# Kernel tuning notes

Measured on AMD Instinct MI355X. Metric: run time of the kernel, lower is better.

## Reference

```python
import jax, jax.numpy as jnp
import numpy as np

B, S, E = 2, 2048, 2048
H, W = 16, 256  # num_heads, window_size
D = E // H      # head_dim = 128


def setup_inputs() -> dict:
    key = jax.random.key(0)
    ks = jax.random.split(key, 9)
    s = 1.0 / np.sqrt(E)
    return {
        "x": jax.random.normal(ks[0], (B, S, E), dtype=jnp.float32),
        "Wq": jax.random.normal(ks[1], (E, E), dtype=jnp.float32) * s,
        "bq": jax.random.normal(ks[2], (E,), dtype=jnp.float32) * 0.01,
        "Wk": jax.random.normal(ks[3], (E, E), dtype=jnp.float32) * s,
        "bk": jax.random.normal(ks[4], (E,), dtype=jnp.float32) * 0.01,
        "Wv": jax.random.normal(ks[5], (E, E), dtype=jnp.float32) * s,
        "bv": jax.random.normal(ks[6], (E,), dtype=jnp.float32) * 0.01,
        "Wo": jax.random.normal(ks[7], (E, E), dtype=jnp.float32) * s,
        "bo": jax.random.normal(ks[8], (E,), dtype=jnp.float32) * 0.01,
    }


def reference(x, Wq, bq, Wk, bk, Wv, bv, Wo, bo):
    Bsz, Sl, _ = x.shape
    # projections -> [B, H, S, D]
    def proj(Wt, bt):
        return (x @ Wt + bt).reshape(Bsz, Sl, H, D).transpose(0, 2, 1, 3)
    q = proj(Wq, bq)
    k = proj(Wk, bk)
    v = proj(Wv, bv)
    # scores [B, H, S, S]
    scores = jnp.einsum("bhqd,bhkd->bhqk", q, k) / jnp.sqrt(jnp.float32(D))
    # causal sliding-window mask: q_pos - W < k_pos <= q_pos
    q_pos = jnp.arange(Sl)[:, None]
    k_pos = jnp.arange(Sl)[None, :]
    valid = (k_pos <= q_pos) & (k_pos > q_pos - W)
    scores = jnp.where(valid, scores, jnp.float32(-jnp.inf))
    attn = jax.nn.softmax(scores, axis=-1)
    ctx = jnp.einsum("bhqk,bhkd->bhqd", attn, v)
    ctx = ctx.transpose(0, 2, 1, 3).reshape(Bsz, Sl, E)
    out = ctx @ Wo + bo
    return out, k, v
```

## Files before the change

### kernel.cpp

```cpp
#include <hip/hip_runtime.h>
#include <hip/hip_bf16.h>

#define SEQ 2048
#define EMB 2048
#define NH 16
#define WIN 256
#define HD 128
#define KDIM 2048
#define NDIM 2048

typedef __bf16 bf16x8 __attribute__((ext_vector_type(8)));
typedef float f32x4 __attribute__((ext_vector_type(4)));

__device__ __forceinline__ ushort f2bf(float f) {
  unsigned int x = __float_as_uint(f);
  unsigned int r = (x + 0x7fffu + ((x >> 16) & 1u)) >> 16;
  return (ushort)r;
}

__device__ __forceinline__ void gl16(const ushort* g, ushort* l) {
  __builtin_amdgcn_global_load_lds(
      (const __attribute__((address_space(1))) ushort*)g,
      (__attribute__((address_space(3))) ushort*)l, 16, 0, 0);
}

__global__ __launch_bounds__(256) void xconv_kernel(
    const float* __restrict__ x, ushort* __restrict__ xb) {
  size_t i = ((size_t)blockIdx.x * 256 + threadIdx.x) * 8;
  float4 f0 = *(const float4*)&x[i];
  float4 f1 = *(const float4*)&x[i + 4];
  union { ushort u[8]; uint4 v; } pk;
  pk.u[0] = f2bf(f0.x); pk.u[1] = f2bf(f0.y);
  pk.u[2] = f2bf(f0.z); pk.u[3] = f2bf(f0.w);
  pk.u[4] = f2bf(f1.x); pk.u[5] = f2bf(f1.y);
  pk.u[6] = f2bf(f1.z); pk.u[7] = f2bf(f1.w);
  *(uint4*)&xb[i] = pk.v;
}

__global__ __launch_bounds__(256) void wtrans_kernel(
    const float* __restrict__ w0, const float* __restrict__ w1,
    const float* __restrict__ w2, const float* __restrict__ w3,
    ushort* __restrict__ wt) {
  __shared__ __align__(16) float tf[32 * 132];
  const int t = threadIdx.x;
  const int nblk = blockIdx.x, kblk = blockIdx.y, mat = blockIdx.z;
  const float* Wp = mat == 0 ? w0 : mat == 1 ? w1 : mat == 2 ? w2 : w3;
  const int n0 = nblk * 128, k0 = kblk * 32;
#pragma unroll
  for (int p = 0; p < 4; ++p) {
    int kk = (t >> 5) + 8 * p;
    int nn = (t & 31) * 4;
    float4 v = *(const float4*)&Wp[(size_t)(k0 + kk) * NDIM + n0 + nn];
    *(float4*)&tf[kk * 132 + nn] = v;
  }
  __syncthreads();
  ushort* dst = wt + (size_t)mat * ((size_t)NDIM * KDIM) +
                (size_t)(nblk * 64 + kblk) * 4096;
#pragma unroll
  for (int p = 0; p < 2; ++p) {
    int idx = p * 256 + t;
    int r = idx >> 2, cs = idx & 3;
    int c = cs ^ ((r >> 1) & 3);
    union { ushort u[8]; uint4 v; } pk;
#pragma unroll
    for (int j = 0; j < 8; ++j) pk.u[j] = f2bf(tf[(c * 8 + j) * 132 + r]);
    *(uint4*)&dst[idx * 8] = pk.v;
  }
}

template <int MODE>
__global__ __launch_bounds__(256) void gemm_kernel(
    const ushort* __restrict__ Ab, const ushort* __restrict__ Wt,
    const float* __restrict__ b0, const float* __restrict__ b1,
    const float* __restrict__ b2, float* __restrict__ outF,
    ushort* __restrict__ outQ) {
  __shared__ __align__(16) ushort As[128 * 32];
  __shared__ __align__(16) ushort Bs[128 * 32];
  const int t = threadIdx.x;
  const int mblk = blockIdx.x, nblk = blockIdx.y, z = blockIdx.z;
  const int m0 = mblk * 128, n0 = nblk * 128;
  const ushort* wtile = Wt + (size_t)z * ((size_t)NDIM * KDIM) +
                        (size_t)(nblk * 64) * 4096;
  const int lane = t & 63, wid = t >> 6;
  const int l15 = lane & 15, lg = lane >> 4;
  const int wm = wid >> 1, wn = wid & 1;
  f32x4 acc[4][4] = {};

  const int slot0 = wid * 128 + lane;
  const int slot1 = slot0 + 64;
  const int r0 = slot0 >> 2, c0 = (slot0 & 3) ^ ((r0 >> 1) & 3);
  const int r1 = slot1 >> 2, c1 = (slot1 & 3) ^ ((r1 >> 1) & 3);
  const ushort* aS0 = Ab + (size_t)(m0 + r0) * KDIM + c0 * 8;
  const ushort* aS1 = Ab + (size_t)(m0 + r1) * KDIM + c1 * 8;
  const ushort* bS0 = wtile + slot0 * 8;
  const ushort* bS1 = wtile + slot1 * 8;
  ushort* aD0 = &As[(wid * 128) * 8];
  ushort* aD1 = &As[(wid * 128 + 64) * 8];
  ushort* bD0 = &Bs[(wid * 128) * 8];
  ushort* bD1 = &Bs[(wid * 128 + 64) * 8];

  for (int kt = 0; kt < KDIM / 32; ++kt) {
    __syncthreads();
    gl16(aS0, aD0); gl16(aS1, aD1);
    gl16(bS0, bD0); gl16(bS1, bD1);
    aS0 += 32; aS1 += 32; bS0 += 4096; bS1 += 4096;
    __syncthreads();
    bf16x8 af[4], bfr[4];
#pragma unroll
    for (int mf = 0; mf < 4; ++mf) {
      int r = wm * 64 + mf * 16 + l15;
      af[mf] = *(const bf16x8*)&As[r * 32 + ((lg ^ ((r >> 1) & 3)) * 8)];
    }
#pragma unroll
    for (int nf = 0; nf < 4; ++nf) {
      int r = wn * 64 + nf * 16 + l15;
      bfr[nf] = *(const bf16x8*)&Bs[r * 32 + ((lg ^ ((r >> 1) & 3)) * 8)];
    }
#pragma unroll
    for (int mf = 0; mf < 4; ++mf)
#pragma unroll
      for (int nf = 0; nf < 4; ++nf)
        acc[mf][nf] = __builtin_amdgcn_mfma_f32_16x16x32_bf16(
            af[mf], bfr[nf], acc[mf][nf], 0, 0, 0);
  }

  const float* bias = (MODE == 0) ? b0 : (z == 0 ? b0 : z == 1 ? b1 : b2);
#pragma unroll
  for (int nf = 0; nf < 4; ++nf) {
    int nl = wn * 64 + nf * 16 + l15;
    int n = n0 + nl;
    float bv = bias[n];
#pragma unroll
    for (int mf = 0; mf < 4; ++mf) {
#pragma unroll
      for (int r = 0; r < 4; ++r) {
        int m = m0 + wm * 64 + mf * 16 + lg * 4 + r;
        float val = acc[mf][nf][r] + bv;
        if (MODE == 0) {
          outF[(size_t)m * NDIM + n] = val;
        } else {
          int b = m >> 11, s = m & 2047;
          size_t idx = (((size_t)b * NH + nblk) * SEQ + s) * HD + nl;
          if (z == 0) outQ[idx] = f2bf(val);
          else outF[(z == 1 ? 8388608u : 16777216u) + idx] = val;
        }
      }
    }
  }
}

__global__ __launch_bounds__(256) void attn_kernel(
    const ushort* __restrict__ Qb, const float* __restrict__ Kf,
    const float* __restrict__ Vf, ushort* __restrict__ ctx) {
  __shared__ __align__(16) ushort Kl[64 * 128];
  __shared__ __align__(16) ushort Vl[128 * 72];
  __shared__ __align__(16) ushort Pl[4 * 16 * 72];
  const int t = threadIdx.x;
  const int bh = blockIdx.x;
  const int q0 = blockIdx.y * 64;
  const int lane = t & 63, w = t >> 6;
  const int l15 = lane & 15, lg = lane >> 4;
  const int b = bh >> 4, h = bh & 15;
  const ushort* Qbase = Qb + (size_t)bh * SEQ * HD;
  const float* Kbase = Kf + (size_t)bh * SEQ * HD;
  const float* Vbase = Vf + (size_t)bh * SEQ * HD;

  bf16x8 aq[4];
#pragma unroll
  for (int ds = 0; ds < 4; ++ds)
    aq[ds] = *(const bf16x8*)&Qbase[(size_t)(q0 + w * 16 + l15) * HD + ds * 32 + lg * 8];

  f32x4 accc[8] = {};
  float mrow[4], lrow[4];
#pragma unroll
  for (int r = 0; r < 4; ++r) { mrow[r] = -1e30f; lrow[r] = 0.f; }

  int ktlo = (q0 - WIN + 1) >> 6;
  if (ktlo < 0) ktlo = 0;
  const int kthi = q0 >> 6;

  for (int kt = ktlo; kt <= kthi; ++kt) {
    __syncthreads();
#pragma unroll
    for (int p = 0; p < 4; ++p) {
      int idx = p * 256 + t;
      int row = idx >> 4, cs = idx & 15;
      int c = cs ^ (row & 7);
      const float* sp = &Kbase[(size_t)(kt * 64 + row) * HD + c * 8];
      float4 f0 = *(const float4*)sp;
      float4 f1 = *(const float4*)(sp + 4);
      union { ushort u[8]; uint4 v; } pk;
      pk.u[0] = f2bf(f0.x); pk.u[1] = f2bf(f0.y);
      pk.u[2] = f2bf(f0.z); pk.u[3] = f2bf(f0.w);
      pk.u[4] = f2bf(f1.x); pk.u[5] = f2bf(f1.y);
      pk.u[6] = f2bf(f1.z); pk.u[7] = f2bf(f1.w);
      *(uint4*)&Kl[row * 128 + cs * 8] = pk.v;
    }
#pragma unroll
    for (int p = 0; p < 4; ++p) {
      int idx = p * 256 + t;
      int key = idx & 63, dc = idx >> 6;
      const float* sp = &Vbase[(size_t)(kt * 64 + key) * HD + dc * 8];
      float4 f0 = *(const float4*)sp;
      float4 f1 = *(const float4*)(sp + 4);
      Vl[(dc * 8 + 0) * 72 + key] = f2bf(f0.x);
      Vl[(dc * 8 + 1) * 72 + key] = f2bf(f0.y);
      Vl[(dc * 8 + 2) * 72 + key] = f2bf(f0.z);
      Vl[(dc * 8 + 3) * 72 + key] = f2bf(f0.w);
      Vl[(dc * 8 + 4) * 72 + key] = f2bf(f1.x);
      Vl[(dc * 8 + 5) * 72 + key] = f2bf(f1.y);
      Vl[(dc * 8 + 6) * 72 + key] = f2bf(f1.z);
      Vl[(dc * 8 + 7) * 72 + key] = f2bf(f1.w);
    }
    __syncthreads();

    f32x4 sacc[4] = {};
#pragma unroll
    for (int ds = 0; ds < 4; ++ds) {
#pragma unroll
      for (int kf = 0; kf < 4; ++kf) {
        int key = kf * 16 + l15;
        bf16x8 kb = *(const bf16x8*)&Kl[key * 128 + (((ds * 4 + lg) ^ (key & 7)) * 8)];
        sacc[kf] = __builtin_amdgcn_mfma_f32_16x16x32_bf16(aq[ds], kb, sacc[kf], 0, 0, 0);
      }
    }

    const float scale = 0.08838834764831845f;
    const float L2E = 1.4426950408889634f;
#pragma unroll
    for (int r = 0; r < 4; ++r) {
      int q = q0 + w * 16 + lg * 4 + r;
      float sv[4];
      float mx = -1e30f;
#pragma unroll
      for (int kf = 0; kf < 4; ++kf) {
        int key = kt * 64 + kf * 16 + l15;
        float s = sacc[kf][r] * scale;
        bool valid = (key <= q) && (key + WIN > q);
        s = valid ? s : -1e30f;
        sv[kf] = s;
        mx = fmaxf(mx, s);
      }
      mx = fmaxf(mx, __shfl_xor(mx, 1));
      mx = fmaxf(mx, __shfl_xor(mx, 2));
      mx = fmaxf(mx, __shfl_xor(mx, 4));
      mx = fmaxf(mx, __shfl_xor(mx, 8));
      float mnew = fmaxf(mrow[r], mx);
      float sf = exp2f((mrow[r] - mnew) * L2E);
      float ps = 0.f;
#pragma unroll
      for (int kf = 0; kf < 4; ++kf) {
        float p = (sv[kf] > -1e29f) ? exp2f((sv[kf] - mnew) * L2E) : 0.f;
        ps += p;
        Pl[w * 1152 + (lg * 4 + r) * 72 + kf * 16 + l15] = f2bf(p);
      }
      ps += __shfl_xor(ps, 1);
      ps += __shfl_xor(ps, 2);
      ps += __shfl_xor(ps, 4);
      ps += __shfl_xor(ps, 8);
      lrow[r] = lrow[r] * sf + ps;
      mrow[r] = mnew;
#pragma unroll
      for (int nf = 0; nf < 8; ++nf) accc[nf][r] *= sf;
    }

#pragma unroll
    for (int ks = 0; ks < 2; ++ks) {
      bf16x8 pa = *(const bf16x8*)&Pl[w * 1152 + l15 * 72 + ks * 32 + lg * 8];
#pragma unroll
      for (int nf = 0; nf < 8; ++nf) {
        bf16x8 vb = *(const bf16x8*)&Vl[(nf * 16 + l15) * 72 + ks * 32 + lg * 8];
        accc[nf] = __builtin_amdgcn_mfma_f32_16x16x32_bf16(pa, vb, accc[nf], 0, 0, 0);
      }
    }
  }

#pragma unroll
  for (int r = 0; r < 4; ++r) {
    int q = q0 + w * 16 + lg * 4 + r;
    float inv = 1.0f / lrow[r];
    size_t rowoff = ((size_t)b * SEQ + q) * EMB + (size_t)h * HD;
#pragma unroll
    for (int nf = 0; nf < 8; ++nf)
      ctx[rowoff + nf * 16 + l15] = f2bf(accc[nf][r] * inv);
  }
}

extern "C" void kernel_launch(void* const* d_in, const int* in_sizes, int n_in,
                              void* d_out, int out_size, void* d_ws, size_t ws_size,
                              hipStream_t stream) {
  const float* x  = (const float*)d_in[0];
  const float* Wq = (const float*)d_in[1];
  const float* bq = (const float*)d_in[2];
  const float* Wk = (const float*)d_in[3];
  const float* bk = (const float*)d_in[4];
  const float* Wv = (const float*)d_in[5];
  const float* bv = (const float*)d_in[6];
  const float* Wo = (const float*)d_in[7];
  const float* bo = (const float*)d_in[8];
  float* out = (float*)d_out;
  ushort* ws = (ushort*)d_ws;
  ushort* Wt   = ws;
  ushort* Qb   = ws + 16777216;
  ushort* xb   = ws + 25165824;
  ushort* ctxb = xb;

  xconv_kernel<<<4096, 256, 0, stream>>>(x, xb);
  wtrans_kernel<<<dim3(16, 64, 4), 256, 0, stream>>>(Wq, Wk, Wv, Wo, Wt);
  gemm_kernel<1><<<dim3(32, 16, 3), 256, 0, stream>>>(xb, Wt, bq, bk, bv, out, Qb);
  attn_kernel<<<dim3(32, 32), 256, 0, stream>>>(Qb, out + 8388608, out + 16777216, ctxb);
  gemm_kernel<0><<<dim3(32, 16, 1), 256, 0, stream>>>(ctxb, Wt + (size_t)3 * 4194304,
                                                      bo, nullptr, nullptr, out, nullptr);
}
```

Before: 236.6 us.

## Triple-buffer GEMM K-tiles with 256x128 tiles, 8 waves and block swizzle

Rewrites the projection GEMM as a 256x128 tile with 512 threads and a K-step of 64. A three-stage LDS ring is filled by async global_load_lds with vmcnt waits, so loads overlap MFMA work. The weight pre-transpose now emits a 64-wide K layout with an 8-way XOR swizzle. Blocks are remapped for L2 locality, and s_setprio/s_barrier interleaving is added around the MFMA groups. The cost is about 144KB of LDS per block and more complex synchronisation, and the occupancy hint of 2 blocks may not fit.

```diff
diff --git a/kernel.cpp b/kernel.cpp
--- a/kernel.cpp
+++ b/kernel.cpp
@@ -41,108 +41,153 @@
     const float* __restrict__ w0, const float* __restrict__ w1,
     const float* __restrict__ w2, const float* __restrict__ w3,
     ushort* __restrict__ wt) {
-  __shared__ __align__(16) float tf[32 * 132];
+  __shared__ __align__(16) float tf[64 * 132];
   const int t = threadIdx.x;
   const int nblk = blockIdx.x, kblk = blockIdx.y, mat = blockIdx.z;
   const float* Wp = mat == 0 ? w0 : mat == 1 ? w1 : mat == 2 ? w2 : w3;
-  const int n0 = nblk * 128, k0 = kblk * 32;
-#pragma unroll
-  for (int p = 0; p < 4; ++p) {
-    int kk = (t >> 5) + 8 * p;
-    int nn = (t & 31) * 4;
+  const int n0 = nblk * 128, k0 = kblk * 64;
+#pragma unroll
+  for (int p = 0; p < 8; ++p) {
+    int idx = p * 256 + t;
+    int kk = idx >> 5;
+    int nn = (idx & 31) * 4;
     float4 v = *(const float4*)&Wp[(size_t)(k0 + kk) * NDIM + n0 + nn];
     *(float4*)&tf[kk * 132 + nn] = v;
   }
   __syncthreads();
   ushort* dst = wt + (size_t)mat * ((size_t)NDIM * KDIM) +
-                (size_t)(nblk * 64 + kblk) * 4096;
-#pragma unroll
-  for (int p = 0; p < 2; ++p) {
-    int idx = p * 256 + t;
-    int r = idx >> 2, cs = idx & 3;
-    int c = cs ^ ((r >> 1) & 3);
+                (size_t)(nblk * 32 + kblk) * 8192;
+#pragma unroll
+  for (int p = 0; p < 4; ++p) {
+    int s = p * 256 + t;
+    int r = s >> 3, kc = s & 7;
+    int cg = kc ^ (r & 7);
     union { ushort u[8]; uint4 v; } pk;
 #pragma unroll
-    for (int j = 0; j < 8; ++j) pk.u[j] = f2bf(tf[(c * 8 + j) * 132 + r]);
-    *(uint4*)&dst[idx * 8] = pk.v;
+    for (int j = 0; j < 8; ++j) pk.u[j] = f2bf(tf[(cg * 8 + j) * 132 + r]);
+    *(uint4*)&dst[s * 8] = pk.v;
   }
 }
 
 template <int MODE>
-__global__ __launch_bounds__(256) void gemm_kernel(
+__global__ __launch_bounds__(512, 2) void gemm_kernel(
     const ushort* __restrict__ Ab, const ushort* __restrict__ Wt,
     const float* __restrict__ b0, const float* __restrict__ b1,
     const float* __restrict__ b2, float* __restrict__ outF,
     ushort* __restrict__ outQ) {
-  __shared__ __align__(16) ushort As[128 * 32];
-  __shared__ __align__(16) ushort Bs[128 * 32];
+  __shared__ __align__(16) ushort L[3 * 24576];
   const int t = threadIdx.x;
-  const int mblk = blockIdx.x, nblk = blockIdx.y, z = blockIdx.z;
-  const int m0 = mblk * 128, n0 = nblk * 128;
-  const ushort* wtile = Wt + (size_t)z * ((size_t)NDIM * KDIM) +
-                        (size_t)(nblk * 64) * 4096;
-  const int lane = t & 63, wid = t >> 6;
+  const int w = t >> 6, lane = t & 63;
   const int l15 = lane & 15, lg = lane >> 4;
-  const int wm = wid >> 1, wn = wid & 1;
+  const int wm = w >> 1, wn = w & 1;
+  const int bid = blockIdx.x + (blockIdx.y << 4);
+  const int wkid = (bid & 7) * 32 + (bid >> 3);
+  const int mblk = wkid & 15, nblk = wkid >> 4;
+  const int z = blockIdx.z;
+  const int m0 = mblk * 256, n0 = nblk * 128;
+  const ushort* wz = Wt + (size_t)z * ((size_t)NDIM * KDIM) +
+                     (size_t)nblk * 32 * 8192;
+
+  const ushort* aS[4];
+#pragma unroll
+  for (int j = 0; j < 4; ++j) {
+    int s = j * 512 + t;
+    int r = s >> 3, kc = s & 7;
+    int cg = kc ^ (r & 7);
+    aS[j] = Ab + (size_t)(m0 + r) * KDIM + cg * 8;
+  }
+  const ushort* bS[2];
+#pragma unroll
+  for (int j = 0; j < 2; ++j) bS[j] = wz + (size_t)(j * 512 + t) * 8;
+
   f32x4 acc[4][4] = {};
 
-  const int slot0 = wid * 128 + lane;
-  const int slot1 = slot0 + 64;
-  const int r0 = slot0 >> 2, c0 = (slot0 & 3) ^ ((r0 >> 1) & 3);
-  const int r1 = slot1 >> 2, c1 = (slot1 & 3) ^ ((r1 >> 1) & 3);
-  const ushort* aS0 = Ab + (size_t)(m0 + r0) * KDIM + c0 * 8;
-  const ushort* aS1 = Ab + (size_t)(m0 + r1) * KDIM + c1 * 8;
-  const ushort* bS0 = wtile + slot0 * 8;
-  const ushort* bS1 = wtile + slot1 * 8;
-  ushort* aD0 = &As[(wid * 128) * 8];
-  ushort* aD1 = &As[(wid * 128 + 64) * 8];
-  ushort* bD0 = &Bs[(wid * 128) * 8];
-  ushort* bD1 = &Bs[(wid * 128 + 64) * 8];
-
-  for (int kt = 0; kt < KDIM / 32; ++kt) {
-    __syncthreads();
-    gl16(aS0, aD0); gl16(aS1, aD1);
-    gl16(bS0, bD0); gl16(bS1, bD1);
-    aS0 += 32; aS1 += 32; bS0 += 4096; bS1 += 4096;
-    __syncthreads();
-    bf16x8 af[4], bfr[4];
-#pragma unroll
-    for (int mf = 0; mf < 4; ++mf) {
-      int r = wm * 64 + mf * 16 + l15;
-      af[mf] = *(const bf16x8*)&As[r * 32 + ((lg ^ ((r >> 1) & 3)) * 8)];
-    }
-#pragma unroll
-    for (int nf = 0; nf < 4; ++nf) {
-      int r = wn * 64 + nf * 16 + l15;
-      bfr[nf] = *(const bf16x8*)&Bs[r * 32 + ((lg ^ ((r >> 1) & 3)) * 8)];
-    }
-#pragma unroll
-    for (int mf = 0; mf < 4; ++mf)
-#pragma unroll
-      for (int nf = 0; nf < 4; ++nf)
-        acc[mf][nf] = __builtin_amdgcn_mfma_f32_16x16x32_bf16(
-            af[mf], bfr[nf], acc[mf][nf], 0, 0, 0);
-  }
+#define STAGE(ts, p)                                                     \
+  {                                                                      \
+    ushort* Ad = &L[(p) * 24576 + w * 512];                              \
+    ushort* Bd = &L[(p) * 24576 + 16384 + w * 512];                      \
+    size_t ko = (size_t)(ts) * 64;                                       \
+    size_t bo = (size_t)(ts) * 8192;                                     \
+    gl16(aS[0] + ko, Ad);                                                \
+    gl16(aS[1] + ko, Ad + 4096);                                         \
+    gl16(aS[2] + ko, Ad + 8192);                                         \
+    gl16(aS[3] + ko, Ad + 12288);                                        \
+    gl16(bS[0] + bo, Bd);                                                \
+    gl16(bS[1] + bo, Bd + 4096);                                         \
+  }
+
+  const int NT = KDIM / 64;
+  STAGE(0, 0)
+  STAGE(1, 1)
+
+  for (int tk = 0; tk < NT; ++tk) {
+    asm volatile("s_waitcnt vmcnt(6)\n\ts_barrier" ::: "memory");
+    const int ts = (tk + 2 < NT) ? (tk + 2) : (NT - 1);
+    const int sp = (tk + 2) % 3;
+    STAGE(ts, sp)
+    const ushort* Ar = &L[(tk % 3) * 24576];
+    const ushort* Br = Ar + 16384;
+
+#pragma unroll
+    for (int kk = 0; kk < 2; ++kk) {
+      bf16x8 af[4], bfn[2];
+#pragma unroll
+      for (int mi = 0; mi < 4; ++mi) {
+        int row = wm * 64 + mi * 16 + l15;
+        af[mi] = *(const bf16x8*)&Ar[row * 64 + (((kk * 4 + lg) ^ (row & 7)) * 8)];
+      }
+#pragma unroll
+      for (int ni = 0; ni < 2; ++ni) {
+        int nr = wn * 64 + ni * 16 + l15;
+        bfn[ni] = *(const bf16x8*)&Br[nr * 64 + (((kk * 4 + lg) ^ (nr & 7)) * 8)];
+      }
+      __builtin_amdgcn_s_barrier();
+      __builtin_amdgcn_s_setprio(1);
+#pragma unroll
+      for (int mi = 0; mi < 4; ++mi)
+#pragma unroll
+        for (int ni = 0; ni < 2; ++ni)
+          acc[mi][ni] = __builtin_amdgcn_mfma_f32_16x16x32_bf16(
+              af[mi], bfn[ni], acc[mi][ni], 0, 0, 0);
+      __builtin_amdgcn_s_setprio(0);
+      bf16x8 bf2[2];
+#pragma unroll
+      for (int ni = 0; ni < 2; ++ni) {
+        int nr = wn * 64 + (ni + 2) * 16 + l15;
+        bf2[ni] = *(const bf16x8*)&Br[nr * 64 + (((kk * 4 + lg) ^ (nr & 7)) * 8)];
+      }
+      __builtin_amdgcn_s_barrier();
+      __builtin_amdgcn_s_setprio(1);
+#pragma unroll
+      for (int mi = 0; mi < 4; ++mi)
+#pragma unroll
+        for (int ni = 0; ni < 2; ++ni)
+          acc[mi][ni + 2] = __builtin_amdgcn_mfma_f32_16x16x32_bf16(
+              af[mi], bf2[ni], acc[mi][ni + 2], 0, 0, 0);
+      __builtin_amdgcn_s_setprio(0);
+    }
+  }
+#undef STAGE
 
   const float* bias = (MODE == 0) ? b0 : (z == 0 ? b0 : z == 1 ? b1 : b2);
 #pragma unroll
-  for (int nf = 0; nf < 4; ++nf) {
-    int nl = wn * 64 + nf * 16 + l15;
+  for (int ni = 0; ni < 4; ++ni) {
+    int nl = wn * 64 + ni * 16 + l15;
     int n = n0 + nl;
     float bv = bias[n];
 #pragma unroll
-    for (int mf = 0; mf < 4; ++mf) {
+    for (int mi = 0; mi < 4; ++mi) {
 #pragma unroll
       for (int r = 0; r < 4; ++r) {
-        int m = m0 + wm * 64 + mf * 16 + lg * 4 + r;
-        float val = acc[mf][nf][r] + bv;
+        int m = m0 + wm * 64 + mi * 16 + lg * 4 + r;
+        float val = acc[mi][ni][r] + bv;
         if (MODE == 0) {
           outF[(size_t)m * NDIM + n] = val;
         } else {
           int b = m >> 11, s = m & 2047;
           size_t idx = (((size_t)b * NH + nblk) * SEQ + s) * HD + nl;
           if (z == 0) outQ[idx] = f2bf(val);
-          else outF[(z == 1 ? 8388608u : 16777216u) + idx] = val;
+          else outF[(z == 1 ? (size_t)8388608u : (size_t)16777216u) + idx] = val;
         }
       }
     }
@@ -306,9 +351,9 @@
   ushort* ctxb = xb;
 
   xconv_kernel<<<4096, 256, 0, stream>>>(x, xb);
-  wtrans_kernel<<<dim3(16, 64, 4), 256, 0, stream>>>(Wq, Wk, Wv, Wo, Wt);
-  gemm_kernel<1><<<dim3(32, 16, 3), 256, 0, stream>>>(xb, Wt, bq, bk, bv, out, Qb);
+  wtrans_kernel<<<dim3(16, 32, 4), 256, 0, stream>>>(Wq, Wk, Wv, Wo, Wt);
+  gemm_kernel<1><<<dim3(16, 16, 3), 512, 0, stream>>>(xb, Wt, bq, bk, bv, out, Qb);
   attn_kernel<<<dim3(32, 32), 256, 0, stream>>>(Qb, out + 8388608, out + 16777216, ctxb);
-  gemm_kernel<0><<<dim3(32, 16, 1), 256, 0, stream>>>(ctxb, Wt + (size_t)3 * 4194304,
+  gemm_kernel<0><<<dim3(16, 16, 1), 512, 0, stream>>>(ctxb, Wt + (size_t)3 * 4194304,
                                                       bo, nullptr, nullptr, out, nullptr);
 }
```

After: 238.6 us. About the same (+0.9%).

## Emit bf16 K and transposed V from QKV GEMM; double-buffer attention loads

Applied to the files above, without the earlier changes.

The QKV projection epilogue now also writes bf16 copies of K and a transposed bf16 V into workspace, alongside the fp32 outputs. The attention kernel then stages K and V tiles straight into LDS with async global_load_lds into double buffers, prefetching two tiles ahead under a vmcnt wait plus barrier. This removes per-tile fp32 loads and conversions and the scattered V transpose stores from the attention inner loop, and overlaps loads with MFMA work. In exchange the GEMM epilogue writes extra data, with narrow 8-byte strided stores for transposed V, and LDS use rises.

```diff
diff --git a/kernel.cpp b/kernel.cpp
--- a/kernel.cpp
+++ b/kernel.cpp
@@ -11,6 +11,9 @@
 
 typedef __bf16 bf16x8 __attribute__((ext_vector_type(8)));
 typedef float f32x4 __attribute__((ext_vector_type(4)));
+
+#define MFMA __builtin_amdgcn_mfma_f32_16x16x32_bf16
+#define BAR __builtin_amdgcn_s_barrier
 
 __device__ __forceinline__ ushort f2bf(float f) {
   unsigned int x = __float_as_uint(f);
@@ -73,7 +76,8 @@
     const ushort* __restrict__ Ab, const ushort* __restrict__ Wt,
     const float* __restrict__ b0, const float* __restrict__ b1,
     const float* __restrict__ b2, float* __restrict__ outF,
-    ushort* __restrict__ outQ) {
+    ushort* __restrict__ outQ, ushort* __restrict__ Kbf,
+    ushort* __restrict__ vTb) {
   __shared__ __align__(16) ushort As[128 * 32];
   __shared__ __align__(16) ushort Bs[128 * 32];
   const int t = threadIdx.x;
@@ -120,8 +124,7 @@
     for (int mf = 0; mf < 4; ++mf)
 #pragma unroll
       for (int nf = 0; nf < 4; ++nf)
-        acc[mf][nf] = __builtin_amdgcn_mfma_f32_16x16x32_bf16(
-            af[mf], bfr[nf], acc[mf][nf], 0, 0, 0);
+        acc[mf][nf] = MFMA(af[mf], bfr[nf], acc[mf][nf], 0, 0, 0);
   }
 
   const float* bias = (MODE == 0) ? b0 : (z == 0 ? b0 : z == 1 ? b1 : b2);
@@ -132,17 +135,36 @@
     float bv = bias[n];
 #pragma unroll
     for (int mf = 0; mf < 4; ++mf) {
-#pragma unroll
-      for (int r = 0; r < 4; ++r) {
-        int m = m0 + wm * 64 + mf * 16 + lg * 4 + r;
-        float val = acc[mf][nf][r] + bv;
-        if (MODE == 0) {
-          outF[(size_t)m * NDIM + n] = val;
+      if (MODE == 0) {
+#pragma unroll
+        for (int r = 0; r < 4; ++r) {
+          int m = m0 + wm * 64 + mf * 16 + lg * 4 + r;
+          outF[(size_t)m * NDIM + n] = acc[mf][nf][r] + bv;
+        }
+      } else {
+        int mbase = m0 + wm * 64 + mf * 16 + lg * 4;
+        int b = mbase >> 11, sbase = mbase & 2047;
+        size_t idx0 = (((size_t)b * NH + nblk) * SEQ + sbase) * HD + nl;
+        if (z == 0) {
+#pragma unroll
+          for (int r = 0; r < 4; ++r)
+            outQ[idx0 + (size_t)r * HD] = f2bf(acc[mf][nf][r] + bv);
+        } else if (z == 1) {
+#pragma unroll
+          for (int r = 0; r < 4; ++r) {
+            float val = acc[mf][nf][r] + bv;
+            outF[(size_t)8388608u + idx0 + (size_t)r * HD] = val;
+            Kbf[idx0 + (size_t)r * HD] = f2bf(val);
+          }
         } else {
-          int b = m >> 11, s = m & 2047;
-          size_t idx = (((size_t)b * NH + nblk) * SEQ + s) * HD + nl;
-          if (z == 0) outQ[idx] = f2bf(val);
-          else outF[(z == 1 ? 8388608u : 16777216u) + idx] = val;
+          union { ushort u[4]; uint2 v; } p4;
+#pragma unroll
+          for (int r = 0; r < 4; ++r) {
+            float val = acc[mf][nf][r] + bv;
+            outF[(size_t)16777216u + idx0 + (size_t)r * HD] = val;
+            p4.u[r] = f2bf(val);
+          }
+          *(uint2*)&vTb[(((size_t)b * NH + nblk) * HD + nl) * SEQ + sbase] = p4.v;
         }
       }
     }
@@ -150,11 +172,11 @@
 }
 
 __global__ __launch_bounds__(256) void attn_kernel(
-    const ushort* __restrict__ Qb, const float* __restrict__ Kf,
-    const float* __restrict__ Vf, ushort* __restrict__ ctx) {
-  __shared__ __align__(16) ushort Kl[64 * 128];
-  __shared__ __align__(16) ushort Vl[128 * 72];
-  __shared__ __align__(16) ushort Pl[4 * 16 * 72];
+    const ushort* __restrict__ Qb, const ushort* __restrict__ Kb,
+    const ushort* __restrict__ vT, ushort* __restrict__ ctx) {
+  __shared__ __align__(16) ushort Kl[2][8192];
+  __shared__ __align__(16) ushort Vt[2][8192];
+  __shared__ __align__(16) ushort Pl[4608];
   const int t = threadIdx.x;
   const int bh = blockIdx.x;
   const int q0 = blockIdx.y * 64;
@@ -162,8 +184,32 @@
   const int l15 = lane & 15, lg = lane >> 4;
   const int b = bh >> 4, h = bh & 15;
   const ushort* Qbase = Qb + (size_t)bh * SEQ * HD;
-  const float* Kbase = Kf + (size_t)bh * SEQ * HD;
-  const float* Vbase = Vf + (size_t)bh * SEQ * HD;
+  const ushort* Kbase = Kb + (size_t)bh * SEQ * HD;
+  const ushort* Vbase = vT + (size_t)bh * HD * SEQ;
+
+  const ushort* kS[4];
+  const ushort* vS[4];
+#pragma unroll
+  for (int p = 0; p < 4; ++p) {
+    int s = p * 256 + t;
+    int kr = s >> 4, kc = (s & 15) ^ (kr & 7);
+    kS[p] = Kbase + kr * HD + kc * 8;
+    int vr = s >> 3, vc = (s & 7) ^ (vr & 7);
+    vS[p] = Vbase + vr * SEQ + vc * 8;
+  }
+
+#define ASTAGE(kt, buf)                                                  \
+  {                                                                      \
+    size_t ko = (size_t)(kt) * 8192, vo = (size_t)(kt) * 64;             \
+    gl16(kS[0] + ko, &Kl[buf][(w * 64) * 8]);                            \
+    gl16(kS[1] + ko, &Kl[buf][(256 + w * 64) * 8]);                      \
+    gl16(kS[2] + ko, &Kl[buf][(512 + w * 64) * 8]);                      \
+    gl16(kS[3] + ko, &Kl[buf][(768 + w * 64) * 8]);                      \
+    gl16(vS[0] + vo, &Vt[buf][(w * 64) * 8]);                            \
+    gl16(vS[1] + vo, &Vt[buf][(256 + w * 64) * 8]);                      \
+    gl16(vS[2] + vo, &Vt[buf][(512 + w * 64) * 8]);                      \
+    gl16(vS[3] + vo, &Vt[buf][(768 + w * 64) * 8]);                      \
+  }
 
   bf16x8 aq[4];
 #pragma unroll
@@ -179,40 +225,16 @@
   if (ktlo < 0) ktlo = 0;
   const int kthi = q0 >> 6;
 
+  ASTAGE(ktlo, 0)
+  {
+    int t1 = (ktlo + 1 <= kthi) ? ktlo + 1 : kthi;
+    ASTAGE(t1, 1)
+  }
+
   for (int kt = ktlo; kt <= kthi; ++kt) {
-    __syncthreads();
-#pragma unroll
-    for (int p = 0; p < 4; ++p) {
-      int idx = p * 256 + t;
-      int row = idx >> 4, cs = idx & 15;
-      int c = cs ^ (row & 7);
-      const float* sp = &Kbase[(size_t)(kt * 64 + row) * HD + c * 8];
-      float4 f0 = *(const float4*)sp;
-      float4 f1 = *(const float4*)(sp + 4);
-      union { ushort u[8]; uint4 v; } pk;
-      pk.u[0] = f2bf(f0.x); pk.u[1] = f2bf(f0.y);
-      pk.u[2] = f2bf(f0.z); pk.u[3] = f2bf(f0.w);
-      pk.u[4] = f2bf(f1.x); pk.u[5] = f2bf(f1.y);
-      pk.u[6] = f2bf(f1.z); pk.u[7] = f2bf(f1.w);
-      *(uint4*)&Kl[row * 128 + cs * 8] = pk.v;
-    }
-#pragma unroll
-    for (int p = 0; p < 4; ++p) {
-      int idx = p * 256 + t;
-      int key = idx & 63, dc = idx >> 6;
-      const float* sp = &Vbase[(size_t)(kt * 64 + key) * HD + dc * 8];
-      float4 f0 = *(const float4*)sp;
-      float4 f1 = *(const float4*)(sp + 4);
-      Vl[(dc * 8 + 0) * 72 + key] = f2bf(f0.x);
-      Vl[(dc * 8 + 1) * 72 + key] = f2bf(f0.y);
-      Vl[(dc * 8 + 2) * 72 + key] = f2bf(f0.z);
-      Vl[(dc * 8 + 3) * 72 + key] = f2bf(f0.w);
-      Vl[(dc * 8 + 4) * 72 + key] = f2bf(f1.x);
-      Vl[(dc * 8 + 5) * 72 + key] = f2bf(f1.y);
-      Vl[(dc * 8 + 6) * 72 + key] = f2bf(f1.z);
-      Vl[(dc * 8 + 7) * 72 + key] = f2bf(f1.w);
-    }
-    __syncthreads();
+    const int buf = (kt - ktlo) & 1;
+    asm volatile("s_waitcnt vmcnt(8)" ::: "memory");
+    BAR();
 
     f32x4 sacc[4] = {};
 #pragma unroll
@@ -220,8 +242,8 @@
 #pragma unroll
       for (int kf = 0; kf < 4; ++kf) {
         int key = kf * 16 + l15;
-        bf16x8 kb = *(const bf16x8*)&Kl[key * 128 + (((ds * 4 + lg) ^ (key & 7)) * 8)];
-        sacc[kf] = __builtin_amdgcn_mfma_f32_16x16x32_bf16(aq[ds], kb, sacc[kf], 0, 0, 0);
+        bf16x8 kb = *(const bf16x8*)&Kl[buf][key * 128 + (((ds * 4 + lg) ^ (key & 7)) * 8)];
+        sacc[kf] = MFMA(aq[ds], kb, sacc[kf], 0, 0, 0);
       }
     }
 
@@ -269,11 +291,19 @@
       bf16x8 pa = *(const bf16x8*)&Pl[w * 1152 + l15 * 72 + ks * 32 + lg * 8];
 #pragma unroll
       for (int nf = 0; nf < 8; ++nf) {
-        bf16x8 vb = *(const bf16x8*)&Vl[(nf * 16 + l15) * 72 + ks * 32 + lg * 8];
-        accc[nf] = __builtin_amdgcn_mfma_f32_16x16x32_bf16(pa, vb, accc[nf], 0, 0, 0);
-      }
-    }
-  }
+        int vr = nf * 16 + l15;
+        bf16x8 vb = *(const bf16x8*)&Vt[buf][vr * 64 + (((ks * 4 + lg) ^ (vr & 7)) * 8)];
+        accc[nf] = MFMA(pa, vb, accc[nf], 0, 0, 0);
+      }
+    }
+
+    BAR();
+    {
+      int ts = (kt + 2 <= kthi) ? kt + 2 : kthi;
+      ASTAGE(ts, buf)
+    }
+  }
+#undef ASTAGE
 
 #pragma unroll
   for (int r = 0; r < 4; ++r) {
@@ -302,13 +332,17 @@
   ushort* ws = (ushort*)d_ws;
   ushort* Wt   = ws;
   ushort* Qb   = ws + 16777216;
-  ushort* xb   = ws + 25165824;
+  ushort* Kbf  = ws + 25165824;
+  ushort* vTb  = ws + 33554432;
+  ushort* xb   = ws + 41943040;
   ushort* ctxb = xb;
 
   xconv_kernel<<<4096, 256, 0, stream>>>(x, xb);
   wtrans_kernel<<<dim3(16, 64, 4), 256, 0, stream>>>(Wq, Wk, Wv, Wo, Wt);
-  gemm_kernel<1><<<dim3(32, 16, 3), 256, 0, stream>>>(xb, Wt, bq, bk, bv, out, Qb);
-  attn_kernel<<<dim3(32, 32), 256, 0, stream>>>(Qb, out + 8388608, out + 16777216, ctxb);
-  gemm_kernel<0><<<dim3(32, 16, 1), 256, 0, stream>>>(ctxb, Wt + (size_t)3 * 4194304,
-                                                      bo, nullptr, nullptr, out, nullptr);
-}
+  gemm_kernel<1><<<dim3(32, 16, 3), 256, 0, stream>>>(xb, Wt, bq, bk, bv, out,
+                                                      Qb, Kbf, vTb);
+  attn_kernel<<<dim3(32, 32), 256, 0, stream>>>(Qb, Kbf, vTb, ctxb);
+  gemm_kernel<0><<<dim3(32, 16, 1), 256, 0, stream>>>(
+      ctxb, Wt + (size_t)3 * 4194304, bo, nullptr, nullptr, out, nullptr,
+      nullptr, nullptr);
+}
```

Result: slower. 248.3 us (+4.9%).
